# Kernel tuning notes

Measured on AMD Instinct MI355X. Metric: run time of the kernel, lower is better.

Reference implementation:

```python
import jax, jax.numpy as jnp
import numpy as np

RADIUS = 3
NPATCH = 9          # patch_sampling_num
DROP_RATE = 0.1
TEMP = 0.5
BW = 1.0            # band_width
K, STRIDE, PAD = 7, 2, 3          # conv params (kernel_size, stride, padding)
POOL_K, POOL_S, POOL_P = 3, 2, 1  # maxpool params
OUTDIM = 64


def _compute_mask(x_old, out_shape):
    """Replicates Info_Dropout's no_grad mask construction."""
    B, C, H, W = x_old.shape
    pl = PAD + RADIUS
    pr = PAD + RADIUS + 1
    padded = jnp.pad(x_old, ((0, 0), (0, 0), (pl, pr), (pl, pr)))
    hd = H + 2 * PAD  # spatial extent of the sliced region (torch: [radius:-radius-1])

    # torch.randint offsets in [-radius, radius]; concrete ints (fixed seed)
    rng = np.random.default_rng(0)
    si = rng.integers(-RADIUS, RADIUS + 1, NPATCH)
    sj = rng.integers(-RADIUS, RADIUS + 1, NPATCH)

    base = padded[:, :, RADIUS:RADIUS + hd, RADIUS:RADIUS + hd]
    dists = []
    for i, j in zip(si, sj):  # fixed small loop over 9 sampled patch offsets
        shifted = padded[:, :, RADIUS + i:RADIUS + i + hd, RADIUS + j:RADIUS + j + hd]
        dists.append(((base - shifted) ** 2).sum(axis=1))  # sum over indim channels
    distance = jnp.stack(dists, axis=1)  # (B, 9, hd, hd)

    # all-ones depthwise KxK stride-S conv == per-channel box sum
    distance = jax.lax.reduce_window(
        distance, 0.0, jax.lax.add,
        (1, 1, K, K), (1, 1, STRIDE, STRIDE), 'VALID')
    distance = jnp.exp(-distance / distance.mean() / 2.0 / (BW ** 2))

    # all-ones 1x1 conv 9->outdim == sum over 9 channels, replicated
    prob = (distance.sum(axis=1, keepdims=True) / NPATCH) ** (1.0 / TEMP)  # (B,1,h,w)
    prob = jnp.broadcast_to(prob, (B, OUTDIM) + prob.shape[2:])

    # prob = -maxpool(-prob) == min-pool; torch maxpool pads with -inf
    prob = -jax.lax.reduce_window(
        -prob, -jnp.inf, jax.lax.max,
        (1, 1, POOL_K, POOL_K), (1, 1, POOL_S, POOL_S),
        [(0, 0), (0, 0), (POOL_P, POOL_P), (POOL_P, POOL_P)])
    prob = prob / prob.sum(axis=(-2, -1), keepdims=True)

    Bo, Co, h, w = out_shape
    nsamp = int(DROP_RATE * h * w)
    flat = prob.reshape(Bo * Co, h * w)
    logits = jnp.log(flat + 1e-8)  # multinomial(prob + 1e-8) with replacement
    key = jax.random.key(42)
    choice = jax.random.categorical(key, logits, axis=-1, shape=(nsamp, Bo * Co)).T  # (BC, nsamp)
    mask = jnp.ones((Bo * Co, h * w), flat.dtype)
    mask = mask.at[jnp.arange(Bo * Co)[:, None], choice].set(0.0)
    return mask.reshape(out_shape)


def setup_inputs() -> dict:
    key = jax.random.key(0)
    k1, k2 = jax.random.split(key)
    x_old = jax.random.normal(k1, (32, 3, 224, 224), dtype=jnp.float32)
    x = jax.random.normal(k2, (32, 64, 56, 56), dtype=jnp.float32)
    return {"x_old": x_old, "x": x}


def reference(x_old, x):
    mask = _compute_mask(x_old, x.shape)
    return x * mask
```

## Files before the change

kernel.cpp:

```cpp
#include <hip/hip_runtime.h>
#include <math.h>
#include <stdint.h>

#pragma clang fp contract(off)

#define NDIST   3612672
#define NPMAP   401408
#define NPOOL   100352
#define NSAMP_T 641024
#define NMEANB  882

__device__ __align__(16) float g_dist[NDIST];
__device__ __align__(16) float g_pmap[NPMAP];
__device__ __align__(16) float g_pooled[NPOOL];
__device__ __align__(16) float g_logits[NPOOL];
__device__ float g_partial[NMEANB];
__device__ float g_rowsum[32];
__device__ float g_lmax[32];
__device__ float g_mean[1];
__device__ int   g_sij[18];

__device__ __forceinline__ uint32_t ss_hash(uint32_t value, uint32_t& hc) {
  value ^= hc; hc *= 0x931e8875u; value *= hc; value ^= value >> 16; return value;
}
__device__ __forceinline__ uint32_t ss_mix(uint32_t x, uint32_t y) {
  uint32_t r = x * 0xca01f9ddu - y * 0x4973f715u;
  r ^= r >> 16; return r;
}

__global__ void k_rng() {
  if (threadIdx.x != 0 || blockIdx.x != 0) return;
  uint32_t pool[4];
  uint32_t hc = 0x43b0d7e5u;
  for (int i = 0; i < 4; ++i) pool[i] = ss_hash(0u, hc);
  for (int is = 0; is < 4; ++is)
    for (int id = 0; id < 4; ++id)
      if (is != id) pool[id] = ss_mix(pool[id], ss_hash(pool[is], hc));
  uint32_t hb = 0x8b51f9ddu;
  uint32_t w[8];
  for (int i = 0; i < 8; ++i) {
    uint32_t dv = pool[i & 3];
    dv ^= hb; hb *= 0x58f38dedu; dv *= hb; dv ^= dv >> 16; w[i] = dv;
  }
  uint64_t gs[4];
  for (int i = 0; i < 4; ++i) gs[i] = (uint64_t)w[2*i] | ((uint64_t)w[2*i+1] << 32);
  const __uint128_t MUL = (((__uint128_t)0x2360ED051FC65DA4ull) << 64) | 0x4385DF649FCCF645ull;
  __uint128_t initstate = (((__uint128_t)gs[0]) << 64) | gs[1];
  __uint128_t initseq   = (((__uint128_t)gs[2]) << 64) | gs[3];
  __uint128_t inc   = (initseq << 1) | 1;
  __uint128_t state = 0;
  state = state * MUL + inc;
  state += initstate;
  state = state * MUL + inc;

  bool has32 = false; uint32_t saved32 = 0;
  auto next32 = [&]() -> uint32_t {
    if (has32) { has32 = false; return saved32; }
    state = state * MUL + inc;
    uint64_t xo = (uint64_t)(state >> 64) ^ (uint64_t)state;
    uint32_t rot = (uint32_t)(state >> 122) & 63u;
    uint64_t v = (xo >> rot) | (xo << ((64u - rot) & 63u));
    has32 = true; saved32 = (uint32_t)(v >> 32);
    return (uint32_t)v;
  };

  for (int k = 0; k < 18; ++k) {
    uint64_t m = (uint64_t)next32() * 7ull;
    uint32_t leftover = (uint32_t)m;
    if (leftover < 7u) {
      while (leftover < 4u) { m = (uint64_t)next32() * 7ull; leftover = (uint32_t)m; }
    }
    g_sij[k] = (int)(uint32_t)(m >> 32) - 3;
  }
}

__global__ __launch_bounds__(256) void k_dist(const float* __restrict__ xold) {
  int idx = blockIdx.x * 256 + threadIdx.x;
  if (idx >= NDIST) return;
  int ox = idx % 112; int tt = idx / 112;
  int oy = tt % 112;  tt /= 112;
  int p = tt % 9;     int b = tt / 9;
  int si = g_sij[p], sj = g_sij[9 + p];
  const float* xb = xold + (size_t)b * 3 * 224 * 224;
  float acc = 0.f;
  for (int kh = 0; kh < 7; ++kh) {
    int hb = 2 * oy + kh - 3;
    int hs = hb + si;
    for (int kw = 0; kw < 7; ++kw) {
      int wb = 2 * ox + kw - 3;
      int wsf = wb + sj;
      float s = 0.f;
      for (int c = 0; c < 3; ++c) {
        const float* xc = xb + c * 224 * 224;
        float bv = (hb >= 0 && hb < 224 && wb >= 0 && wb < 224) ? xc[hb * 224 + wb] : 0.f;
        float sv = (hs >= 0 && hs < 224 && wsf >= 0 && wsf < 224) ? xc[hs * 224 + wsf] : 0.f;
        float d = bv - sv;
        s = s + d * d;
      }
      acc = acc + s;
    }
  }
  g_dist[idx] = acc;
}

__global__ __launch_bounds__(256) void k_mean1() {
  __shared__ float red[256];
  int base = blockIdx.x * 4096;
  float acc = 0.f;
  #pragma unroll
  for (int i = 0; i < 4; ++i) {
    float4 v = *(const float4*)(g_dist + base + threadIdx.x * 4 + i * 1024);
    acc = acc + v.x + v.y + v.z + v.w;
  }
  red[threadIdx.x] = acc;
  __syncthreads();
  for (int s = 128; s > 0; s >>= 1) {
    if (threadIdx.x < s) red[threadIdx.x] += red[threadIdx.x + s];
    __syncthreads();
  }
  if (threadIdx.x == 0) g_partial[blockIdx.x] = red[0];
}
__global__ void k_mean2() {
  if (threadIdx.x != 0 || blockIdx.x != 0) return;
  float acc = 0.f;
  for (int i = 0; i < NMEANB; ++i) acc = acc + g_partial[i];
  g_mean[0] = acc / 3612672.0f;
}

__global__ __launch_bounds__(256) void k_prob1() {
  int idx = blockIdx.x * 256 + threadIdx.x;
  if (idx >= NPMAP) return;
  int xy = idx % 12544; int b = idx / 12544;
  float m = g_mean[0];
  float ssum = 0.f;
  for (int p = 0; p < 9; ++p) {
    float d = g_dist[(size_t)(b * 9 + p) * 12544 + xy];
    float t = (-d / m) / 2.0f;
    float e = expf(t);
    ssum = ssum + e;
  }
  float q = ssum / 9.0f;
  g_pmap[idx] = q * q;
}

__global__ __launch_bounds__(256) void k_pool() {
  int idx = blockIdx.x * 256 + threadIdx.x;
  if (idx >= NPOOL) return;
  int ox = idx % 56; int tt = idx / 56;
  int oy = tt % 56;  int b = tt / 56;
  float mn = INFINITY;
  for (int kh = 0; kh < 3; ++kh) {
    int y = 2 * oy - 1 + kh; if (y < 0 || y >= 112) continue;
    for (int kw = 0; kw < 3; ++kw) {
      int x = 2 * ox - 1 + kw; if (x < 0 || x >= 112) continue;
      mn = fminf(mn, g_pmap[(size_t)(b * 112 + y) * 112 + x]);
    }
  }
  g_pooled[idx] = mn;
}

__global__ void k_norm1() {
  int b = threadIdx.x;
  if (b >= 32 || blockIdx.x != 0) return;
  const float* P = g_pooled + b * 3136;
  float s = 0.f;
  for (int i = 0; i < 3136; ++i) s = s + P[i];
  g_rowsum[b] = s;
}

__global__ __launch_bounds__(256) void k_norm2() {
  __shared__ float red[4];
  int b = blockIdx.x;
  float s = g_rowsum[b];
  const float* P = g_pooled + b * 3136;
  float lm = -INFINITY;
  for (int i = threadIdx.x; i < 3136; i += 256) {
    float fl = P[i] / s;
    float lg = logf(fl + 1e-8f);
    g_logits[b * 3136 + i] = lg;
    lm = fmaxf(lm, lg);
  }
  #pragma unroll
  for (int off = 32; off; off >>= 1) lm = fmaxf(lm, __shfl_xor(lm, off));
  int wid = threadIdx.x >> 6;
  if ((threadIdx.x & 63) == 0) red[wid] = lm;
  __syncthreads();
  if (threadIdx.x == 0)
    g_lmax[b] = fmaxf(fmaxf(red[0], red[1]), fmaxf(red[2], red[3]));
}

__global__ __launch_bounds__(256) void k_copy(const float4* __restrict__ x, float4* __restrict__ out) {
  int i = blockIdx.x * 256 + threadIdx.x;
  out[i] = x[i];
}

__device__ __forceinline__ uint32_t rotl32(uint32_t x, int r) { return __builtin_rotateleft32(x, r); }
__device__ __forceinline__ void threefry2x32(uint32_t x0, uint32_t x1, uint32_t& o0, uint32_t& o1) {
  const uint32_t ks0 = 0u, ks1 = 42u, ks2 = 0x1BD11BDAu ^ 0u ^ 42u;
  x0 += ks0; x1 += ks1;
#define TFR(r) { x0 += x1; x1 = rotl32(x1, (r)); x1 ^= x0; }
  TFR(13) TFR(15) TFR(26) TFR(6)  x0 += ks1; x1 += ks2 + 1u;
  TFR(17) TFR(29) TFR(16) TFR(24) x0 += ks2; x1 += ks0 + 2u;
  TFR(13) TFR(15) TFR(26) TFR(6)  x0 += ks0; x1 += ks1 + 3u;
  TFR(17) TFR(29) TFR(16) TFR(24) x0 += ks1; x1 += ks2 + 4u;
  TFR(13) TFR(15) TFR(26) TFR(6)  x0 += ks2; x1 += ks0 + 5u;
#undef TFR
  o0 = x0; o1 = x1;
}

__device__ __forceinline__ uint32_t random_bits_at(uint32_t idx) {
  uint32_t o0, o1; threefry2x32(0u, idx, o0, o1);
  return o0 ^ o1;
}

#define TF7_R(S) \
  "v_add_u32 %0, %0, %1\n\t" "v_add_u32 %2, %2, %3\n\t" "v_add_u32 %4, %4, %5\n\t" \
  "v_add_u32 %6, %6, %7\n\t" "v_add_u32 %8, %8, %9\n\t" "v_add_u32 %10, %10, %11\n\t" \
  "v_add_u32 %12, %12, %13\n\t" \
  "v_alignbit_b32 %1, %1, %1, " S "\n\t" "v_alignbit_b32 %3, %3, %3, " S "\n\t" \
  "v_alignbit_b32 %5, %5, %5, " S "\n\t" "v_alignbit_b32 %7, %7, %7, " S "\n\t" \
  "v_alignbit_b32 %9, %9, %9, " S "\n\t" "v_alignbit_b32 %11, %11, %11, " S "\n\t" \
  "v_alignbit_b32 %13, %13, %13, " S "\n\t" \
  "v_xor_b32 %1, %1, %0\n\t" "v_xor_b32 %3, %3, %2\n\t" "v_xor_b32 %5, %5, %4\n\t" \
  "v_xor_b32 %7, %7, %6\n\t" "v_xor_b32 %9, %9, %8\n\t" "v_xor_b32 %11, %11, %10\n\t" \
  "v_xor_b32 %13, %13, %12\n\t"
#define TF7_GX TF7_R("19") TF7_R("17") TF7_R("6") TF7_R("26")
#define TF7_GY TF7_R("15") TF7_R("3") TF7_R("16") TF7_R("8")
#define TF7_I0(L) \
  "v_add_u32 %0, " L ", %0\n\t" "v_add_u32 %2, " L ", %2\n\t" "v_add_u32 %4, " L ", %4\n\t" \
  "v_add_u32 %6, " L ", %6\n\t" "v_add_u32 %8, " L ", %8\n\t" "v_add_u32 %10, " L ", %10\n\t" \
  "v_add_u32 %12, " L ", %12\n\t"
#define TF7_I1(L) \
  "v_add_u32 %1, " L ", %1\n\t" "v_add_u32 %3, " L ", %3\n\t" "v_add_u32 %5, " L ", %5\n\t" \
  "v_add_u32 %7, " L ", %7\n\t" "v_add_u32 %9, " L ", %9\n\t" "v_add_u32 %11, " L ", %11\n\t" \
  "v_add_u32 %13, " L ", %13\n\t"

__device__ __forceinline__ void tf7_sept(uint32_t base,
                                         uint32_t& o0, uint32_t& o1, uint32_t& o2,
                                         uint32_t& o3, uint32_t& o4, uint32_t& o5, uint32_t& o6) {
  uint32_t a0 = 0u, a1 = base + 42u;
  uint32_t b0 = 0u, b1 = base + 106u;
  uint32_t c0 = 0u, c1 = base + 170u;
  uint32_t d0 = 0u, d1 = base + 234u;
  uint32_t e0 = 0u, e1 = base + 298u;
  uint32_t f0 = 0u, f1 = base + 362u;
  uint32_t g0 = 0u, g1 = base + 426u;
  asm(TF7_GX
      TF7_I0("42")          TF7_I1("0x1bd11bf1")
      TF7_GY
      TF7_I0("0x1bd11bf0")  TF7_I1("2")
      TF7_GX
      TF7_I1("45")
      TF7_GY
      TF7_I0("42")          TF7_I1("0x1bd11bf4")
      TF7_GX
      TF7_I0("0x1bd11bf0")  TF7_I1("5")
      "v_xor_b32 %0, %0, %1\n\t" "v_xor_b32 %2, %2, %3\n\t" "v_xor_b32 %4, %4, %5\n\t"
      "v_xor_b32 %6, %6, %7\n\t" "v_xor_b32 %8, %8, %9\n\t" "v_xor_b32 %10, %10, %11\n\t"
      "v_xor_b32 %12, %12, %13"
      : "+v"(a0), "+v"(a1), "+v"(b0), "+v"(b1), "+v"(c0), "+v"(c1), "+v"(d0), "+v"(d1),
        "+v"(e0), "+v"(e1), "+v"(f0), "+v"(f1), "+v"(g0), "+v"(g1));
  o0 = a0; o1 = b0; o2 = c0; o3 = d0; o4 = e0; o5 = f0; o6 = g0;
}

__device__ __forceinline__ float gumbel_ocml(uint32_t mant) {
  float uni;
  if (mant == 0u) uni = 1.17549435e-38f;
  else uni = __uint_as_float(0x3f800000u | mant) - 1.0f;
  float l1 = logf(uni);
  float n1 = -l1;
  float l2 = logf(n1);
  return -l2;
}


#define TOP3_UPD(x, jj) { \
  bool g1 = (x) > w1; \
  bool g2 = (x) > w2; \
  uint32_t nw3; asm("v_med3_u32 %0, %1, %2, %3" : "=v"(nw3) : "v"(x), "v"(w2), "v"(w3)); \
  uint32_t nw2; asm("v_med3_u32 %0, %1, %2, %3" : "=v"(nw2) : "v"(x), "v"(w1), "v"(w2)); \
  w3 = nw3; w2 = nw2; \
  j2 = g1 ? j1 : (g2 ? (jj) : j2); \
  j1 = g1 ? (jj) : j1; \
  w1 = max(w1, (x)); }

__global__ __launch_bounds__(256) void k_samp(float* __restrict__ out) {
  int lane  = threadIdx.x & 63;
  int t = blockIdx.x * 4 + (threadIdx.x >> 6);
  int r = t & 2047;
  int b = __builtin_amdgcn_readfirstlane(r >> 6);
  const float* L = g_logits + b * 3136;
  float Lmx = g_lmax[b];
  uint32_t vbase = (uint32_t)t * 3136u;

  uint32_t w1, w2 = 0u, w3 = 0u; int j1, j2 = 0;
  uint32_t vidx = vbase + (uint32_t)lane;
  {
    uint32_t x0, x1, x2, x3, x4, x5, x6;
    tf7_sept(vidx, x0, x1, x2, x3, x4, x5, x6);
    w1 = x0; j1 = lane;
    TOP3_UPD(x1, lane + 64)
    TOP3_UPD(x2, lane + 128)
    TOP3_UPD(x3, lane + 192)
    TOP3_UPD(x4, lane + 256)
    TOP3_UPD(x5, lane + 320)
    TOP3_UPD(x6, lane + 384)
    vidx += 448u;
  }
  int jb = lane + 448;
  #pragma unroll 1
  for (int B = 1; B < 7; ++B) {
    uint32_t x0, x1, x2, x3, x4, x5, x6;
    tf7_sept(vidx, x0, x1, x2, x3, x4, x5, x6);
    TOP3_UPD(x0, jb)
    TOP3_UPD(x1, jb + 64)
    TOP3_UPD(x2, jb + 128)
    TOP3_UPD(x3, jb + 192)
    TOP3_UPD(x4, jb + 256)
    TOP3_UPD(x5, jb + 320)
    TOP3_UPD(x6, jb + 384)
    vidx += 448u; jb += 448;
  }

  float val1 = L[j1] + gumbel_ocml(w1 >> 9);
  float T0 = val1;
  #pragma unroll
  for (int off = 32; off; off >>= 1) T0 = fmaxf(T0, __shfl_xor(T0, off));

  float Tp = T0 - Lmx - 1e-3f;
  uint32_t mthr = 0u;
  if (Tp > -80.0f) {
    float u_thr = expf(-expf(-Tp));
    int mi = (int)(u_thr * 8388608.0f) - 8;
    mthr = mi > 0 ? (uint32_t)mi : 0u;
  }
  uint32_t B0 = mthr << 9;

  float bestV; int bestJ;
  if (w1 >= B0) { bestV = val1; bestJ = j1; }
  else          { bestV = -INFINITY; bestJ = 0x7fffffff; }

  if (__any(w2 >= B0)) {
    if (w2 >= B0) {
      float v2 = L[j2] + gumbel_ocml(w2 >> 9);
      if (v2 > bestV || (v2 == bestV && j2 < bestJ)) { bestV = v2; bestJ = j2; }
    }
  }
  bool f3 = (w3 >= B0) || (B0 == 0u);
  if (__any(f3)) {
    if (f3) {
      uint32_t vi = vbase + (uint32_t)lane;
      #pragma unroll 1
      for (int k = 0; k < 49; ++k) {
        uint32_t x = random_bits_at(vi);
        if (x >= B0) {
          int j = lane + (k << 6);
          float v = L[j] + gumbel_ocml(x >> 9);
          if (v > bestV || (v == bestV && j < bestJ)) { bestV = v; bestJ = j; }
        }
        vi += 64u;
      }
    }
  }

  #pragma unroll
  for (int off = 32; off; off >>= 1) {
    float ov = __shfl_xor(bestV, off);
    int   oj = __shfl_xor(bestJ, off);
    if (ov > bestV || (ov == bestV && oj < bestJ)) { bestV = ov; bestJ = oj; }
  }
  if (lane == 0) out[(size_t)r * 3136 + (size_t)bestJ] = 0.0f;
}

extern "C" void kernel_launch(void* const* d_in, const int* in_sizes, int n_in,
                              void* d_out, int out_size, void* d_ws, size_t ws_size,
                              hipStream_t stream) {
  (void)in_sizes; (void)n_in; (void)d_ws; (void)ws_size; (void)out_size;
  const float* x_old = (const float*)d_in[0];
  const float* x     = (const float*)d_in[1];
  float* out = (float*)d_out;

  k_rng  <<<1,     64, 0, stream>>>();
  k_dist <<<14112, 256, 0, stream>>>(x_old);
  k_mean1<<<NMEANB,256, 0, stream>>>();
  k_mean2<<<1,     64, 0, stream>>>();
  k_prob1<<<1568,  256, 0, stream>>>();
  k_pool <<<392,   256, 0, stream>>>();
  k_norm1<<<1,     64, 0, stream>>>();
  k_norm2<<<32,   256, 0, stream>>>();
  k_copy <<<6272,  256, 0, stream>>>((const float4*)x, (float4*)out);
  k_samp <<<160256, 256, 0, stream>>>(out);
}
```

Measured before the change: 4.602 ms.

## Keep all 49 random words in registers and drop top-3 tracking and regeneration

Stores every per-lane random draw in a 49-entry register array instead of tracking only the top three values. The threshold pass then scans the cached values instead of regenerating the Threefry bits when the third-best passes, and the top-3 update shrinks to a top-1 update. This removes repeated RNG computation and med3 bookkeeping, but adds about 49 live VGPRs per thread. That can cut occupancy or cause spills, and the fully unrolled loop runs 49 wave-wide any-checks.

```diff
diff --git a/kernel.cpp b/kernel.cpp
--- a/kernel.cpp
+++ b/kernel.cpp
@@ -274,15 +274,22 @@
 }
 
 
-#define TOP3_UPD(x, jj) { \
-  bool g1 = (x) > w1; \
-  bool g2 = (x) > w2; \
-  uint32_t nw3; asm("v_med3_u32 %0, %1, %2, %3" : "=v"(nw3) : "v"(x), "v"(w2), "v"(w3)); \
-  uint32_t nw2; asm("v_med3_u32 %0, %1, %2, %3" : "=v"(nw2) : "v"(x), "v"(w1), "v"(w2)); \
-  w3 = nw3; w2 = nw2; \
-  j2 = g1 ? j1 : (g2 ? (jj) : j2); \
-  j1 = g1 ? (jj) : j1; \
+#define TOP1_UPD(x, jj) { \
+  bool g = (x) > w1; \
+  j1 = g ? (jj) : j1; \
   w1 = max(w1, (x)); }
+
+#define SEPT_BLOCK(B) { \
+  tf7_sept(vb + (uint32_t)((B) * 448), \
+           bb[(B)*7], bb[(B)*7+1], bb[(B)*7+2], bb[(B)*7+3], \
+           bb[(B)*7+4], bb[(B)*7+5], bb[(B)*7+6]); \
+  TOP1_UPD(bb[(B)*7],   lane + (B)*448) \
+  TOP1_UPD(bb[(B)*7+1], lane + (B)*448 + 64) \
+  TOP1_UPD(bb[(B)*7+2], lane + (B)*448 + 128) \
+  TOP1_UPD(bb[(B)*7+3], lane + (B)*448 + 192) \
+  TOP1_UPD(bb[(B)*7+4], lane + (B)*448 + 256) \
+  TOP1_UPD(bb[(B)*7+5], lane + (B)*448 + 320) \
+  TOP1_UPD(bb[(B)*7+6], lane + (B)*448 + 384) }
 
 __global__ __launch_bounds__(256) void k_samp(float* __restrict__ out) {
   int lane  = threadIdx.x & 63;
@@ -291,36 +298,26 @@
   int b = __builtin_amdgcn_readfirstlane(r >> 6);
   const float* L = g_logits + b * 3136;
   float Lmx = g_lmax[b];
-  uint32_t vbase = (uint32_t)t * 3136u;
-
-  uint32_t w1, w2 = 0u, w3 = 0u; int j1, j2 = 0;
-  uint32_t vidx = vbase + (uint32_t)lane;
+  uint32_t vb = (uint32_t)t * 3136u + (uint32_t)lane;
+
+  uint32_t bb[49];
+  uint32_t w1; int j1;
   {
-    uint32_t x0, x1, x2, x3, x4, x5, x6;
-    tf7_sept(vidx, x0, x1, x2, x3, x4, x5, x6);
-    w1 = x0; j1 = lane;
-    TOP3_UPD(x1, lane + 64)
-    TOP3_UPD(x2, lane + 128)
-    TOP3_UPD(x3, lane + 192)
-    TOP3_UPD(x4, lane + 256)
-    TOP3_UPD(x5, lane + 320)
-    TOP3_UPD(x6, lane + 384)
-    vidx += 448u;
-  }
-  int jb = lane + 448;
-  #pragma unroll 1
-  for (int B = 1; B < 7; ++B) {
-    uint32_t x0, x1, x2, x3, x4, x5, x6;
-    tf7_sept(vidx, x0, x1, x2, x3, x4, x5, x6);
-    TOP3_UPD(x0, jb)
-    TOP3_UPD(x1, jb + 64)
-    TOP3_UPD(x2, jb + 128)
-    TOP3_UPD(x3, jb + 192)
-    TOP3_UPD(x4, jb + 256)
-    TOP3_UPD(x5, jb + 320)
-    TOP3_UPD(x6, jb + 384)
-    vidx += 448u; jb += 448;
-  }
+    tf7_sept(vb, bb[0], bb[1], bb[2], bb[3], bb[4], bb[5], bb[6]);
+    w1 = bb[0]; j1 = lane;
+    TOP1_UPD(bb[1], lane + 64)
+    TOP1_UPD(bb[2], lane + 128)
+    TOP1_UPD(bb[3], lane + 192)
+    TOP1_UPD(bb[4], lane + 256)
+    TOP1_UPD(bb[5], lane + 320)
+    TOP1_UPD(bb[6], lane + 384)
+  }
+  SEPT_BLOCK(1)
+  SEPT_BLOCK(2)
+  SEPT_BLOCK(3)
+  SEPT_BLOCK(4)
+  SEPT_BLOCK(5)
+  SEPT_BLOCK(6)
 
   float val1 = L[j1] + gumbel_ocml(w1 >> 9);
   float T0 = val1;
@@ -336,29 +333,15 @@
   }
   uint32_t B0 = mthr << 9;
 
-  float bestV; int bestJ;
-  if (w1 >= B0) { bestV = val1; bestJ = j1; }
-  else          { bestV = -INFINITY; bestJ = 0x7fffffff; }
-
-  if (__any(w2 >= B0)) {
-    if (w2 >= B0) {
-      float v2 = L[j2] + gumbel_ocml(w2 >> 9);
-      if (v2 > bestV || (v2 == bestV && j2 < bestJ)) { bestV = v2; bestJ = j2; }
-    }
-  }
-  bool f3 = (w3 >= B0) || (B0 == 0u);
-  if (__any(f3)) {
-    if (f3) {
-      uint32_t vi = vbase + (uint32_t)lane;
-      #pragma unroll 1
-      for (int k = 0; k < 49; ++k) {
-        uint32_t x = random_bits_at(vi);
-        if (x >= B0) {
-          int j = lane + (k << 6);
-          float v = L[j] + gumbel_ocml(x >> 9);
-          if (v > bestV || (v == bestV && j < bestJ)) { bestV = v; bestJ = j; }
-        }
-        vi += 64u;
+  float bestV = -INFINITY; int bestJ = 0x7fffffff;
+  #pragma unroll
+  for (int k = 0; k < 49; ++k) {
+    bool pass = (bb[k] >= B0);
+    if (__any(pass)) {
+      if (pass) {
+        int jj = lane + (k << 6);
+        float v = L[jj] + gumbel_ocml(bb[k] >> 9);
+        if (v > bestV || (v == bestV && jj < bestJ)) { bestV = v; bestJ = jj; }
       }
     }
   }
```

Result: faster. 4.395 ms (-4.5%).
